# Performance work log

Measured on AMD Instinct MI355X. Metric: run time of the kernel, lower is better.

## Reference

```python
import jax, jax.numpy as jnp
import numpy as np

VOCAB, E = 100000, 128
B, S = 256, 512

def setup_inputs() -> dict:
    key = jax.random.key(0)
    k1, k2, k3, k4, k5, k6 = jax.random.split(key, 6)
    x = jax.random.randint(k1, (B, S), 0, VOCAB, dtype=jnp.int64 if jax.config.jax_enable_x64 else jnp.int32)
    emb = jax.random.normal(k2, (VOCAB, E), dtype=jnp.float32) * 0.02
    Wq = jax.random.normal(k3, (E, 1), dtype=jnp.float32) * (1.0 / np.sqrt(E))
    bq = jax.random.normal(k4, (1,), dtype=jnp.float32) * 0.01
    Wm = jax.random.normal(k5, (E, 2), dtype=jnp.float32) * (1.0 / np.sqrt(E))
    bm = jax.random.normal(k6, (2,), dtype=jnp.float32) * 0.01
    return {"x": x, "emb": emb, "Wq": Wq, "bq": bq, "Wm": Wm, "bm": bm}

def reference(x, emb, Wq, bq, Wm, bm):
    embed_x = emb[x]                                  # [B,S,E] gather
    q = embed_x @ Wq + bq                             # [B,S,1] query projection
    # torch.einsum('ijk,ijk->ij') broadcasts q's size-1 k dim:
    log_p = q[..., 0] * embed_x.sum(axis=-1)          # [B,S]
    p = jax.nn.softmax(log_p, axis=1)                 # softmax over sequence
    t_hat = jnp.einsum('bs,bse->be', p, embed_x)      # attention-weighted pool [B,E]
    return jax.nn.relu(t_hat @ Wm + bm)               # [B,2]
```

## Files before the change

kernel.cpp:

```cpp
#include <hip/hip_runtime.h>
#include <math.h>

#define EDIM 128
#define BB   256
#define SS   512
#define NWAVE 16
#define BLOCK (NWAVE * 64)

template<int CTRL>
__device__ __forceinline__ float dpp_add(float v) {
    int r = __builtin_amdgcn_update_dpp(0, __float_as_int(v), CTRL, 0xF, 0xF, true);
    return v + __int_as_float(r);
}

__device__ __forceinline__ float rowsum16(float v) {
    v = dpp_add<0xB1>(v);
    v = dpp_add<0x4E>(v);
    v = dpp_add<0x124>(v);
    v = dpp_add<0x128>(v);
    return v;
}

__global__ __launch_bounds__(BLOCK)
void fused_embed_attn_kernel(const int* __restrict__ x,
                             const float* __restrict__ emb,
                             const float* __restrict__ Wq,
                             const float* __restrict__ bq,
                             const float* __restrict__ Wm,
                             const float* __restrict__ bm,
                             float* __restrict__ out)
{
    const int b    = blockIdx.x;
    const int tid  = threadIdx.x;
    const int wave = tid >> 6;
    const int lane = tid & 63;
    const int row  = lane >> 4;
    const int slot = lane & 15;
    const int d0   = slot * 8;

    const float4 wq0 = *reinterpret_cast<const float4*>(Wq + d0);
    const float4 wq1 = *reinterpret_cast<const float4*>(Wq + d0 + 4);
    const float  bq0 = bq[0];

    const int tbase = b * SS + wave * 32 + row * 8;
    const int4 ia = *reinterpret_cast<const int4*>(x + tbase);
    const int4 ib = *reinterpret_cast<const int4*>(x + tbase + 4);
    const int idx[8] = {ia.x, ia.y, ia.z, ia.w, ib.x, ib.y, ib.z, ib.w};

    float4 e0[8], e1[8];
    #pragma unroll
    for (int i = 0; i < 8; ++i) {
        const float* rp = emb + (size_t)idx[i] * EDIM + d0;
        e0[i] = *reinterpret_cast<const float4*>(rp);
        e1[i] = *reinterpret_cast<const float4*>(rp + 4);
    }

    float m = -INFINITY, Z = 0.f;
    float acc[8] = {0.f, 0.f, 0.f, 0.f, 0.f, 0.f, 0.f, 0.f};

    #pragma unroll
    for (int i = 0; i < 8; ++i) {
        float q = e0[i].x * wq0.x + e0[i].y * wq0.y + e0[i].z * wq0.z + e0[i].w * wq0.w
                + e1[i].x * wq1.x + e1[i].y * wq1.y + e1[i].z * wq1.z + e1[i].w * wq1.w;
        float s = e0[i].x + e0[i].y + e0[i].z + e0[i].w
                + e1[i].x + e1[i].y + e1[i].z + e1[i].w;
        q = rowsum16(q);
        s = rowsum16(s);
        const float lp = (q + bq0) * s;

        const float mn = fmaxf(m, lp);
        const float al = __expf(m - mn);
        const float w  = __expf(lp - mn);
        Z = Z * al + w;
        acc[0] = acc[0] * al + w * e0[i].x;  acc[1] = acc[1] * al + w * e0[i].y;
        acc[2] = acc[2] * al + w * e0[i].z;  acc[3] = acc[3] * al + w * e0[i].w;
        acc[4] = acc[4] * al + w * e1[i].x;  acc[5] = acc[5] * al + w * e1[i].y;
        acc[6] = acc[6] * al + w * e1[i].z;  acc[7] = acc[7] * al + w * e1[i].w;
        m = mn;
    }

    float m1 = fmaxf(m, __shfl_xor(m, 16));
    const float M  = fmaxf(m1, __shfl_xor(m1, 32));
    const float sc = __expf(m - M);
    float Zs = Z * sc;
    Zs += __shfl_xor(Zs, 16);
    Zs += __shfl_xor(Zs, 32);
    #pragma unroll
    for (int j = 0; j < 8; ++j) {
        float a = acc[j] * sc;
        a += __shfl_xor(a, 16);
        a += __shfl_xor(a, 32);
        acc[j] = a;
    }

    __shared__ float sm[NWAVE];
    __shared__ float szv[NWAVE];
    __shared__ float sacc[NWAVE][EDIM];

    if (row == 0) {
        *reinterpret_cast<float4*>(&sacc[wave][d0])     = make_float4(acc[0], acc[1], acc[2], acc[3]);
        *reinterpret_cast<float4*>(&sacc[wave][d0 + 4]) = make_float4(acc[4], acc[5], acc[6], acc[7]);
        if (slot == 0) { sm[wave] = M; szv[wave] = Zs; }
    }
    __syncthreads();

    if (tid < 64) {
        float Mb = sm[0];
        #pragma unroll
        for (int w = 1; w < NWAVE; ++w) Mb = fmaxf(Mb, sm[w]);
        float zt = 0.f, tv0 = 0.f, tv1 = 0.f;
        #pragma unroll
        for (int w = 0; w < NWAVE; ++w) {
            const float s2 = __expf(sm[w] - Mb);
            zt += szv[w] * s2;
            const float2 a2 = *reinterpret_cast<const float2*>(&sacc[w][2 * tid]);
            tv0 += a2.x * s2;
            tv1 += a2.y * s2;
        }
        const float t0 = tv0 / zt, t1 = tv1 / zt;
        const float4 wm = *reinterpret_cast<const float4*>(Wm + 4 * tid);
        float c0 = t0 * wm.x + t1 * wm.z;
        float c1 = t0 * wm.y + t1 * wm.w;
        #pragma unroll
        for (int off = 32; off >= 1; off >>= 1) {
            c0 += __shfl_xor(c0, off);
            c1 += __shfl_xor(c1, off);
        }
        if (tid == 0) {
            out[b * 2 + 0] = fmaxf(c0 + bm[0], 0.f);
            out[b * 2 + 1] = fmaxf(c1 + bm[1], 0.f);
        }
    }
}

extern "C" void kernel_launch(void* const* d_in, const int* in_sizes, int n_in,
                              void* d_out, int out_size, void* d_ws, size_t ws_size,
                              hipStream_t stream) {
    const int*   x   = (const int*)  d_in[0];
    const float* emb = (const float*)d_in[1];
    const float* Wq  = (const float*)d_in[2];
    const float* bq  = (const float*)d_in[3];
    const float* Wm  = (const float*)d_in[4];
    const float* bm  = (const float*)d_in[5];
    float* out = (float*)d_out;

    hipLaunchKernelGGL(fused_embed_attn_kernel, dim3(BB), dim3(BLOCK), 0,
                       stream, x, emb, Wq, bq, Wm, bm, out);
}
```

Measured before the change: 96.71 us.

## Split each sequence across two blocks with a separate merge kernel

The fused kernel becomes a partial kernel that launches two blocks per batch row, each handling half of the sequence with 4 tokens per thread group instead of 8. Each block writes its max, normaliser and unnormalised pooled vector to workspace, and a small second kernel merges the two halves and applies the output projection. The per-token online-softmax rescaling is replaced by a max-then-sum over the 4 tokens. The aim is more blocks and more memory-level parallelism for the gather on a 256-CU GPU, at the cost of a second launch and a workspace round trip.

```diff
diff --git a/kernel.cpp b/kernel.cpp
--- a/kernel.cpp
+++ b/kernel.cpp
@@ -6,6 +6,7 @@
 #define SS   512
 #define NWAVE 16
 #define BLOCK (NWAVE * 64)
+#define TPG   4
 
 template<int CTRL>
 __device__ __forceinline__ float dpp_add(float v) {
@@ -21,16 +22,16 @@
     return v;
 }
 
-__global__ __launch_bounds__(BLOCK)
-void fused_embed_attn_kernel(const int* __restrict__ x,
-                             const float* __restrict__ emb,
-                             const float* __restrict__ Wq,
-                             const float* __restrict__ bq,
-                             const float* __restrict__ Wm,
-                             const float* __restrict__ bm,
-                             float* __restrict__ out)
+__global__ __launch_bounds__(BLOCK, 8)
+void partial_kernel(const int* __restrict__ x,
+                    const float* __restrict__ emb,
+                    const float* __restrict__ Wq,
+                    const float* __restrict__ bq,
+                    float* __restrict__ ws)
 {
-    const int b    = blockIdx.x;
+    const int part = blockIdx.x;
+    const int b    = part >> 1;
+    const int half = part & 1;
     const int tid  = threadIdx.x;
     const int wave = tid >> 6;
     const int lane = tid & 63;
@@ -42,41 +43,42 @@
     const float4 wq1 = *reinterpret_cast<const float4*>(Wq + d0 + 4);
     const float  bq0 = bq[0];
 
-    const int tbase = b * SS + wave * 32 + row * 8;
-    const int4 ia = *reinterpret_cast<const int4*>(x + tbase);
-    const int4 ib = *reinterpret_cast<const int4*>(x + tbase + 4);
-    const int idx[8] = {ia.x, ia.y, ia.z, ia.w, ib.x, ib.y, ib.z, ib.w};
+    const int g     = wave * 4 + row;
+    const int tbase = b * SS + half * 256 + g * TPG;
+    const int4 iv   = *reinterpret_cast<const int4*>(x + tbase);
+    const int idx[TPG] = {iv.x, iv.y, iv.z, iv.w};
 
-    float4 e0[8], e1[8];
+    float4 e0[TPG], e1[TPG];
     #pragma unroll
-    for (int i = 0; i < 8; ++i) {
+    for (int i = 0; i < TPG; ++i) {
         const float* rp = emb + (size_t)idx[i] * EDIM + d0;
         e0[i] = *reinterpret_cast<const float4*>(rp);
         e1[i] = *reinterpret_cast<const float4*>(rp + 4);
     }
 
-    float m = -INFINITY, Z = 0.f;
-    float acc[8] = {0.f, 0.f, 0.f, 0.f, 0.f, 0.f, 0.f, 0.f};
-
+    float lp[TPG];
     #pragma unroll
-    for (int i = 0; i < 8; ++i) {
+    for (int i = 0; i < TPG; ++i) {
         float q = e0[i].x * wq0.x + e0[i].y * wq0.y + e0[i].z * wq0.z + e0[i].w * wq0.w
                 + e1[i].x * wq1.x + e1[i].y * wq1.y + e1[i].z * wq1.z + e1[i].w * wq1.w;
         float s = e0[i].x + e0[i].y + e0[i].z + e0[i].w
                 + e1[i].x + e1[i].y + e1[i].z + e1[i].w;
         q = rowsum16(q);
         s = rowsum16(s);
-        const float lp = (q + bq0) * s;
+        lp[i] = (q + bq0) * s;
+    }
+    float m = fmaxf(fmaxf(lp[0], lp[1]), fmaxf(lp[2], lp[3]));
 
-        const float mn = fmaxf(m, lp);
-        const float al = __expf(m - mn);
-        const float w  = __expf(lp - mn);
-        Z = Z * al + w;
-        acc[0] = acc[0] * al + w * e0[i].x;  acc[1] = acc[1] * al + w * e0[i].y;
-        acc[2] = acc[2] * al + w * e0[i].z;  acc[3] = acc[3] * al + w * e0[i].w;
-        acc[4] = acc[4] * al + w * e1[i].x;  acc[5] = acc[5] * al + w * e1[i].y;
-        acc[6] = acc[6] * al + w * e1[i].z;  acc[7] = acc[7] * al + w * e1[i].w;
-        m = mn;
+    float Z = 0.f;
+    float acc[8] = {0.f, 0.f, 0.f, 0.f, 0.f, 0.f, 0.f, 0.f};
+    #pragma unroll
+    for (int i = 0; i < TPG; ++i) {
+        const float w = __expf(lp[i] - m);
+        Z += w;
+        acc[0] += w * e0[i].x;  acc[1] += w * e0[i].y;
+        acc[2] += w * e0[i].z;  acc[3] += w * e0[i].w;
+        acc[4] += w * e1[i].x;  acc[5] += w * e1[i].y;
+        acc[6] += w * e1[i].z;  acc[7] += w * e1[i].w;
     }
 
     float m1 = fmaxf(m, __shfl_xor(m, 16));
@@ -104,32 +106,54 @@
     }
     __syncthreads();
 
-    if (tid < 64) {
+    if (tid < EDIM) {
         float Mb = sm[0];
         #pragma unroll
         for (int w = 1; w < NWAVE; ++w) Mb = fmaxf(Mb, sm[w]);
-        float zt = 0.f, tv0 = 0.f, tv1 = 0.f;
+        float zt = 0.f, tv = 0.f;
         #pragma unroll
         for (int w = 0; w < NWAVE; ++w) {
             const float s2 = __expf(sm[w] - Mb);
             zt += szv[w] * s2;
-            const float2 a2 = *reinterpret_cast<const float2*>(&sacc[w][2 * tid]);
-            tv0 += a2.x * s2;
-            tv1 += a2.y * s2;
+            tv += sacc[w][tid] * s2;
         }
-        const float t0 = tv0 / zt, t1 = tv1 / zt;
-        const float4 wm = *reinterpret_cast<const float4*>(Wm + 4 * tid);
-        float c0 = t0 * wm.x + t1 * wm.z;
-        float c1 = t0 * wm.y + t1 * wm.w;
-        #pragma unroll
-        for (int off = 32; off >= 1; off >>= 1) {
-            c0 += __shfl_xor(c0, off);
-            c1 += __shfl_xor(c1, off);
-        }
-        if (tid == 0) {
-            out[b * 2 + 0] = fmaxf(c0 + bm[0], 0.f);
-            out[b * 2 + 1] = fmaxf(c1 + bm[1], 0.f);
-        }
+        ws[1024 + part * EDIM + tid] = tv;
+        if (tid == 0) { ws[part] = Mb; ws[512 + part] = zt; }
+    }
+}
+
+__global__ __launch_bounds__(64)
+void merge_kernel(const float* __restrict__ ws,
+                  const float* __restrict__ Wm,
+                  const float* __restrict__ bm,
+                  float* __restrict__ out)
+{
+    const int b    = blockIdx.x;
+    const int lane = threadIdx.x;
+
+    const float m0 = ws[b * 2],       m1 = ws[b * 2 + 1];
+    const float z0 = ws[512 + b * 2], z1 = ws[512 + b * 2 + 1];
+    const float M  = fmaxf(m0, m1);
+    const float s0 = __expf(m0 - M);
+    const float s1 = __expf(m1 - M);
+    const float zt = z0 * s0 + z1 * s1;
+
+    const float2 a0 = *reinterpret_cast<const float2*>(ws + 1024 + (b * 2)     * EDIM + 2 * lane);
+    const float2 a1 = *reinterpret_cast<const float2*>(ws + 1024 + (b * 2 + 1) * EDIM + 2 * lane);
+    const float t0 = (a0.x * s0 + a1.x * s1) / zt;
+    const float t1 = (a0.y * s0 + a1.y * s1) / zt;
+
+    const float4 wm = *reinterpret_cast<const float4*>(Wm + 4 * lane);
+    float c0 = t0 * wm.x + t1 * wm.z;
+    float c1 = t0 * wm.y + t1 * wm.w;
+    #pragma unroll
+    for (int off = 32; off >= 1; off >>= 1) {
+        c0 += __shfl_xor(c0, off);
+        c1 += __shfl_xor(c1, off);
+    }
+    if (lane == 0) {
+        out[b * 2 + 0] = fmaxf(c0 + bm[0], 0.f);
+        out[b * 2 + 1] = fmaxf(c1 + bm[1], 0.f);
     }
 }
 
@@ -143,7 +167,10 @@
     const float* Wm  = (const float*)d_in[4];
     const float* bm  = (const float*)d_in[5];
     float* out = (float*)d_out;
+    float* ws  = (float*)d_ws;
 
-    hipLaunchKernelGGL(fused_embed_attn_kernel, dim3(BB), dim3(BLOCK), 0,
-                       stream, x, emb, Wq, bq, Wm, bm, out);
+    hipLaunchKernelGGL(partial_kernel, dim3(2 * BB), dim3(BLOCK), 0, stream,
+                       x, emb, Wq, bq, ws);
+    hipLaunchKernelGGL(merge_kernel, dim3(BB), dim3(64), 0, stream,
+                       ws, Wm, bm, out);
 }
```

Result: slower. 138.5 us (+43.2%).
